# Kernel optimization log

Measured on AMD Instinct MI355X. Metric: run time of the kernel, lower is better.

Reference implementation:

```python
import jax, jax.numpy as jnp
import numpy as np

B, N, D = 1, 4096, 512
H, HD = 8, 64
NBINS = 512
CAND = 64
SCALE = 1.0 / np.sqrt(HD)
MAX_NORM = 1.0 - 1e-5
TWO_PI = 2.0 * np.pi


def _project(x):
    # Poincare-ball style projection: clip L2 norm of each point to MAX_NORM.
    n = jnp.sqrt(jnp.sum(x * x, axis=-1, keepdims=True))
    s = jnp.minimum(1.0, MAX_NORM / jnp.maximum(n, 1e-12))
    return x * s


def _bins(x):
    # Deterministic geometric binning (DavisCache stand-in): quantize the
    # angle of the first two coordinates into NBINS bins.
    ang = jnp.arctan2(x[..., 1], x[..., 0])  # (-pi, pi]
    b = jnp.floor((ang / TWO_PI + 0.5) * NBINS)
    return jnp.clip(b, 0, NBINS - 1).astype(jnp.int32)


def setup_inputs() -> dict:
    key0 = jax.random.key(0)
    ks = jax.random.split(key0, 12)
    w = 0.02  # typical init scale for projection weights
    return {
        "query": jax.random.normal(ks[0], (B, N, D), dtype=jnp.float32),
        "key": jax.random.normal(ks[1], (B, N, D), dtype=jnp.float32),
        "value": jax.random.normal(ks[2], (B, N, D), dtype=jnp.float32),
        "Wq": jax.random.normal(ks[3], (D, D), dtype=jnp.float32) * w,
        "bq": jnp.zeros((D,), dtype=jnp.float32),
        "Wk": jax.random.normal(ks[4], (D, D), dtype=jnp.float32) * w,
        "bk": jnp.zeros((D,), dtype=jnp.float32),
        "Wv": jax.random.normal(ks[5], (D, D), dtype=jnp.float32) * w,
        "bv": jnp.zeros((D,), dtype=jnp.float32),
        "Wo": jax.random.normal(ks[6], (D, D), dtype=jnp.float32) * w,
        "bo": jnp.zeros((D,), dtype=jnp.float32),
    }


def reference(query, key, value, Wq, bq, Wk, bk, Wv, bv, Wo, bo):
    Bq, Nq, Dm = query.shape
    Nk = key.shape[1]
    # projections + split heads -> (B, H, N, HD)
    q = (query @ Wq.T + bq).reshape(Bq, Nq, H, HD).transpose(0, 2, 1, 3)
    k = (key @ Wk.T + bk).reshape(Bq, Nk, H, HD).transpose(0, 2, 1, 3)
    v = (value @ Wv.T + bv).reshape(Bq, Nk, H, HD).transpose(0, 2, 1, 3)
    q = _project(q)
    k = _project(k)

    # geometric binning; candidate keys for a query are those whose bin is
    # within radius 1 of the query's bin (neighboring_bins, radius=1).
    qb = _bins(q)  # (B, H, Nq) int32
    kb = _bins(k)  # (B, H, Nk) int32
    mask = jnp.abs(qb[..., :, None] - kb[..., None, :]) <= 1  # (B,H,Nq,Nk)
    # fallback: if a query has no candidates, attend over all keys
    any_valid = jnp.any(mask, axis=-1, keepdims=True)
    eff = jnp.where(any_valid, mask, True)
    # keep only the first CAND candidates per query (by key index)
    rank = jnp.cumsum(eff.astype(jnp.int32), axis=-1) - 1
    sel = eff & (rank < CAND)

    scores = jnp.einsum("bhqd,bhkd->bhqk", q, k) * SCALE
    scores = jnp.where(sel, scores, -jnp.inf)
    attn = jax.nn.softmax(scores, axis=-1)  # dropout p=0.0 (eval mode)
    out = jnp.einsum("bhqk,bhkd->bhqd", attn, v)

    out = out.transpose(0, 2, 1, 3).reshape(Bq, Nq, Dm)
    return out @ Wo.T + bo
```

## Files before the change

kernel.cpp:

```cpp
#include <hip/hip_runtime.h>
#include <math.h>

typedef unsigned short u16;
typedef __attribute__((ext_vector_type(8))) short v8bf;
typedef __attribute__((ext_vector_type(4))) float f32x4;

#define N_TOK 4096
#define DMODEL 512
#define NHEAD 8
#define HDIM 64
#define CANDN 64
#define NBINS 512
#define BINCAP 64
#define QCAP 128
#define ATT_SCALE 0.125f
#define MAX_NORM_F 0.99999f

__device__ __forceinline__ u16 f2bf(float f) {
  union { float f; unsigned int i; } v; v.f = f;
  unsigned int x = v.i;
  return (u16)((x + 0x7fffu + ((x >> 16) & 1u)) >> 16);
}
__device__ __forceinline__ uint4 pack8v(const float4 x0, const float4 x1) {
  union { u16 h[8]; uint4 u; } r;
  r.h[0] = f2bf(x0.x); r.h[1] = f2bf(x0.y); r.h[2] = f2bf(x0.z); r.h[3] = f2bf(x0.w);
  r.h[4] = f2bf(x1.x); r.h[5] = f2bf(x1.y); r.h[6] = f2bf(x1.z); r.h[7] = f2bf(x1.w);
  return r.u;
}

__global__ __launch_bounds__(256) void fused1_kernel(
    const float* __restrict__ query, const float* __restrict__ key_,
    const float* __restrict__ value,
    const float* __restrict__ Wq, const float* __restrict__ Wk,
    const float* __restrict__ Wv,
    const float* __restrict__ bq, const float* __restrict__ bk,
    const float* __restrict__ bv,
    int* __restrict__ qb, int* __restrict__ kb, unsigned char* __restrict__ flags,
    int* __restrict__ khist,
    u16* __restrict__ Qb, u16* __restrict__ Kb, u16* __restrict__ Vb)
{
  __shared__ __align__(16) char smem[33024];
  const int blk = blockIdx.x;
  const int tid = threadIdx.x;

  if (blk >= 1280) {
    int4 z4; z4.x = 0; z4.y = 0; z4.z = 0; z4.w = 0;
#pragma unroll
    for (int i = 0; i < 8; ++i) ((int4*)khist)[tid + i * 256] = z4;
    return;
  }

  if (blk >= 512) {
    u16* As = (u16*)smem;
    u16* Ws = (u16*)(smem + 10240);

    const int rel = blk - 512;
    const int z = rel >> 8;
    const int rem = rel & 255;
    const int bm = (rem & 63) * 64;
    const int bn = (rem >> 6) * 128;

    const float* X  = (z == 0) ? query : (z == 1) ? key_ : value;
    const float* WF = (z == 0) ? Wq : (z == 1) ? Wk : Wv;
    const float* bias = (z == 0) ? bq : (z == 1) ? bk : bv;
    u16* O          = (z == 0) ? Qb : (z == 1) ? Kb : Vb;

    const int lane = tid & 63;
    const int wave = tid >> 6;
    const int ra  = tid >> 2;
    const int oa  = (tid & 3) * 8;
    const int wm = (wave & 1) * 32;
    const int wn = (wave >> 1) * 64;
    const int l15 = lane & 15;
    const int quad = lane >> 4;

    f32x4 acc[2][4] = {};

    float4 a0f0 = *(const float4*)(X + (bm + ra) * DMODEL + oa);
    float4 a0f1 = *(const float4*)(X + (bm + ra) * DMODEL + oa + 4);
    float4 w0f0 = *(const float4*)(WF + (bn + ra) * DMODEL + oa);
    float4 w0f1 = *(const float4*)(WF + (bn + ra) * DMODEL + oa + 4);
    float4 w1f0 = *(const float4*)(WF + (bn + ra + 64) * DMODEL + oa);
    float4 w1f1 = *(const float4*)(WF + (bn + ra + 64) * DMODEL + oa + 4);

    for (int kt = 0; kt < DMODEL; kt += 32) {
      const int p = (kt >> 5) & 1;
      *(uint4*)&As[p * 2560 + ra * 40 + oa] = pack8v(a0f0, a0f1);
      *(uint4*)&Ws[p * 5120 + ra * 40 + oa] = pack8v(w0f0, w0f1);
      *(uint4*)&Ws[p * 5120 + (ra + 64) * 40 + oa] = pack8v(w1f0, w1f1);
      __syncthreads();
      if (kt + 32 < DMODEL) {
        a0f0 = *(const float4*)(X + (bm + ra) * DMODEL + kt + 32 + oa);
        a0f1 = *(const float4*)(X + (bm + ra) * DMODEL + kt + 32 + oa + 4);
        w0f0 = *(const float4*)(WF + (bn + ra) * DMODEL + kt + 32 + oa);
        w0f1 = *(const float4*)(WF + (bn + ra) * DMODEL + kt + 32 + oa + 4);
        w1f0 = *(const float4*)(WF + (bn + ra + 64) * DMODEL + kt + 32 + oa);
        w1f1 = *(const float4*)(WF + (bn + ra + 64) * DMODEL + kt + 32 + oa + 4);
      }
      v8bf af[2], bfr[4];
#pragma unroll
      for (int i = 0; i < 2; ++i)
        af[i] = *(const v8bf*)&As[p * 2560 + (wm + i * 16 + l15) * 40 + quad * 8];
#pragma unroll
      for (int j = 0; j < 4; ++j)
        bfr[j] = *(const v8bf*)&Ws[p * 5120 + (wn + j * 16 + l15) * 40 + quad * 8];
#pragma unroll
      for (int i = 0; i < 2; ++i)
#pragma unroll
        for (int j = 0; j < 4; ++j)
          acc[i][j] = __builtin_amdgcn_mfma_f32_16x16x32_bf16(af[i], bfr[j], acc[i][j], 0, 0, 0);
    }

    float bval[4];
#pragma unroll
    for (int j = 0; j < 4; ++j) bval[j] = bias[bn + wn + j * 16 + l15];
    const int h = (bn + wn) >> 6;

#pragma unroll
    for (int i = 0; i < 2; ++i) {
#pragma unroll
      for (int r = 0; r < 4; ++r) {
        const int row = bm + wm + i * 16 + quad * 4 + r;
        float v0 = acc[i][0][r] + bval[0];
        float v1 = acc[i][1][r] + bval[1];
        float v2 = acc[i][2][r] + bval[2];
        float v3 = acc[i][3][r] + bval[3];
        if (z != 2) {
          float ss = v0 * v0 + v1 * v1 + v2 * v2 + v3 * v3;
#pragma unroll
          for (int o = 1; o < 16; o <<= 1) ss += __shfl_xor(ss, o);
          const float s = fminf(1.0f, MAX_NORM_F / fmaxf(sqrtf(ss), 1e-12f));
          v0 *= s; v1 *= s; v2 *= s; v3 *= s;
        }
        const int base = (((h << 12) + row) << 6) + l15;
        O[base +  0] = f2bf(v0); O[base + 16] = f2bf(v1);
        O[base + 32] = f2bf(v2); O[base + 48] = f2bf(v3);
      }
    }
    return;
  }

  float* xs = (float*)smem;
  const int isk  = blk >> 8;
  const int tile = blk & 255;
  const float* X = isk ? key_ : query;
  const float* W = isk ? Wk : Wq;

#pragma unroll
  for (int i = 0; i < 8; ++i) {
    const int flat = i * 1024 + tid * 4;
    const int row = flat >> 9, col = flat & 511;
    *(float4*)&xs[row * 516 + col] = *(const float4*)(X + (tile * 16 + row) * DMODEL + col);
  }
  __syncthreads();

  const int n_local = tid >> 4;
  const int pair = tid & 15;
  const int h = pair >> 1, coord = pair & 1;
  const float* wrow = W + ((h << 6) + coord) * DMODEL;
  const float* xrow = &xs[n_local * 516];

  double c0 = 0.0, c1 = 0.0, c2 = 0.0, c3 = 0.0;
  for (int k = 0; k < DMODEL; k += 4) {
    const float4 xv = *(const float4*)(xrow + k);
    const float4 wv = *(const float4*)(wrow + k);
    c0 = fma((double)xv.x, (double)wv.x, c0);
    c1 = fma((double)xv.y, (double)wv.y, c1);
    c2 = fma((double)xv.z, (double)wv.z, c2);
    c3 = fma((double)xv.w, (double)wv.w, c3);
  }
  const double a = (c0 + c1) + (c2 + c3);
  const double other = __shfl_xor(a, 1);
  if (coord == 0) {
    const double a0 = a, a1 = other;
    const int n = tile * 16 + n_local;
    double ang = atan2(a1, a0);
    double t = (ang / 6.283185307179586 + 0.5) * 512.0;
    int b = (int)floor(t);
    b = b < 0 ? 0 : (b > 511 ? 511 : b);
    (isk ? kb : qb)[(h << 12) + n] = b;

    const double r = sqrt(a0 * a0 + a1 * a1);
    const double dist = fabs(t - nearbyint(t));
    const double margin = fmin(0.45, 3.3e-4 / fmax(r, 1e-30) + 5e-5);
    flags[(isk << 15) | (h << 12) | n] = (dist < margin) ? 1 : 0;
  }
}

__device__ float fdlibm_atanf(float x) {
#pragma clang fp contract(off)
  const float atanhi[4] = {4.6364760399e-01f, 7.8539812565e-01f,
                           9.8279368877e-01f, 1.5707962513e+00f};
  const float atanlo[4] = {5.0121582440e-09f, 3.7748947079e-08f,
                           3.4473217170e-08f, 7.5497894159e-08f};
  const float aT[5] = {3.3333328366e-01f, -1.9999158382e-01f, 1.4253635705e-01f,
                       -1.0648017377e-01f, 6.1687607318e-02f};
  unsigned ix = __float_as_uint(x);
  const unsigned sign = ix >> 31;
  ix &= 0x7fffffffu;
  int id;
  float z, w, s1, s2;
  if (ix >= 0x4c800000u) {
    z = atanhi[3] + 0x1p-120f;
    return sign ? -z : z;
  }
  if (ix < 0x3ee00000u) {
    if (ix < 0x39800000u) return x;
    id = -1;
  } else {
    x = fabsf(x);
    if (ix < 0x3f980000u) {
      if (ix < 0x3f300000u) { id = 0; x = (2.0f * x - 1.0f) / (2.0f + x); }
      else                  { id = 1; x = (x - 1.0f) / (x + 1.0f); }
    } else {
      if (ix < 0x401c0000u) { id = 2; x = (x - 1.5f) / (1.0f + 1.5f * x); }
      else                  { id = 3; x = -1.0f / x; }
    }
  }
  z = x * x;
  w = z * z;
  s1 = z * (aT[0] + w * (aT[2] + w * aT[4]));
  s2 = w * (aT[1] + w * aT[3]);
  if (id < 0) return x - x * (s1 + s2);
  z = atanhi[id] - ((x * (s1 + s2) - atanlo[id]) - x);
  return sign ? -z : z;
}

__device__ float fdlibm_atan2f(float y, float x) {
#pragma clang fp contract(off)
  const float pi = 3.1415927410e+00f, pi_lo = -8.7422776573e-08f;
  const unsigned hx = __float_as_uint(x), hy = __float_as_uint(y);
  if (hx == 0x3f800000u) return fdlibm_atanf(y);
  const unsigned m = ((hy >> 31) & 1u) | ((hx >> 30) & 2u);
  const unsigned ix = hx & 0x7fffffffu, iy = hy & 0x7fffffffu;
  if (iy == 0u) {
    switch (m) { case 0: case 1: return y; case 2: return pi; default: return -pi; }
  }
  if (ix == 0u) return (m & 1u) ? -1.57079637050628662f : 1.57079637050628662f;
  float z;
  if (ix + (26u << 23) < iy) {
    z = 1.57079637050628662f;
    return (m & 1u) ? -z : z;
  }
  if ((m & 2u) && iy + (26u << 23) < ix) z = 0.0f;
  else z = fdlibm_atanf(fabsf(y / x));
  switch (m) {
    case 0: return z;
    case 1: return -z;
    case 2: return pi - (z - pi_lo);
    default: return (z - pi_lo) - pi;
  }
}

__global__ __launch_bounds__(256) void binfix_kernel(
    const float* __restrict__ query, const float* __restrict__ key_,
    const float* __restrict__ Wq, const float* __restrict__ Wk,
    const unsigned char* __restrict__ flags,
    int* __restrict__ qb, int* __restrict__ kb)
{
  __shared__ int wle[64];
  __shared__ int wlc;

  const int tid = threadIdx.x;
  const int slice = blockIdx.x;

  if (tid == 0) wlc = 0;
  __syncthreads();
  if (tid < 128) {
    const int flat = (slice << 7) + tid;
    if (flags[flat]) {
      const int p = atomicAdd(&wlc, 1);
      if (p < 64) wle[p] = flat;
    }
  }
  __syncthreads();
  int nw = wlc; if (nw > 64) nw = 64;
  const int w = tid >> 6, d = tid & 63;
  for (int e = w; e < nw; e += 4) {
    const int flat = wle[e];
    const int n = flat & 4095;
    const int h = (flat >> 12) & 7;
    const int isk = flat >> 15;
    const float* xr = (isk ? key_ : query) + n * DMODEL;
    const float* wr = (isk ? Wk : Wq) + ((h << 6) + d) * DMODEL;
    float acc = 0.0f;
    for (int k = 0; k < DMODEL; k += 16) {
      const float4 xa = *(const float4*)(xr + k);
      const float4 xb = *(const float4*)(xr + k + 4);
      const float4 xc = *(const float4*)(xr + k + 8);
      const float4 xd = *(const float4*)(xr + k + 12);
      const float4 wa = *(const float4*)(wr + k);
      const float4 wb = *(const float4*)(wr + k + 4);
      const float4 wc = *(const float4*)(wr + k + 8);
      const float4 wd = *(const float4*)(wr + k + 12);
      acc = __fmaf_rn(xa.x, wa.x, acc); acc = __fmaf_rn(xa.y, wa.y, acc);
      acc = __fmaf_rn(xa.z, wa.z, acc); acc = __fmaf_rn(xa.w, wa.w, acc);
      acc = __fmaf_rn(xb.x, wb.x, acc); acc = __fmaf_rn(xb.y, wb.y, acc);
      acc = __fmaf_rn(xb.z, wb.z, acc); acc = __fmaf_rn(xb.w, wb.w, acc);
      acc = __fmaf_rn(xc.x, wc.x, acc); acc = __fmaf_rn(xc.y, wc.y, acc);
      acc = __fmaf_rn(xc.z, wc.z, acc); acc = __fmaf_rn(xc.w, wc.w, acc);
      acc = __fmaf_rn(xd.x, wd.x, acc); acc = __fmaf_rn(xd.y, wd.y, acc);
      acc = __fmaf_rn(xd.z, wd.z, acc); acc = __fmaf_rn(xd.w, wd.w, acc);
    }
    {
#pragma clang fp contract(off)
      const float sq = acc * acc;
      float rr[8];
#pragma unroll
      for (int j = 0; j < 8; ++j) rr[j] = __shfl(sq, j);
      for (int i = 8; i < 64; i += 8) {
#pragma unroll
        for (int j = 0; j < 8; ++j) rr[j] += __shfl(sq, i + j);
      }
      const float ss = ((rr[0] + rr[1]) + (rr[2] + rr[3])) +
                       ((rr[4] + rr[5]) + (rr[6] + rr[7]));
      const float nrm = __fsqrt_rn(ss);
      const float s = fminf(1.0f, 0.99999f / fmaxf(nrm, 1e-12f));
      const float c0 = __shfl(acc, 0) * s;
      const float c1 = __shfl(acc, 1) * s;
      const float cr = (float)atan2((double)c1, (double)c0);
      const float fd = fdlibm_atan2f(c1, c0);
      const float tol = fmaxf(fabsf(cr) * 6e-7f, 1e-30f);
      const float ang = (fabsf(fd - cr) <= tol) ? fd : cr;
      const float t = ((ang / 6.2831854820251465f) + 0.5f) * 512.0f;
      int b = (int)floorf(t);
      b = b < 0 ? 0 : (b > 511 ? 511 : b);
      if (d == 0) (isk ? kb : qb)[(h << 12) + n] = b;
    }
  }
}

__global__ __launch_bounds__(256) void bin_hist_kernel(
    const int* __restrict__ kb, const int* __restrict__ qb,
    int* __restrict__ khist, u16* __restrict__ blist,
    int* __restrict__ qhist, u16* __restrict__ qlist)
{
  const int h = blockIdx.x;
  const int type = blockIdx.y;
  const int* src = type ? qb : kb;
  int* hist = type ? qhist : khist;
  u16* list = type ? qlist : blist;
  const int cap = type ? QCAP : BINCAP;

  const int i = blockIdx.z * 256 + threadIdx.x;
  const int b = src[(h << 12) + i];
  const int pos = atomicAdd(&hist[(h << 9) + b], 1);
  if (pos < cap) list[((h << 9) + b) * cap + pos] = (u16)i;
}

__global__ __launch_bounds__(64) void attn_bin_kernel(
    const u16* __restrict__ Qb, const u16* __restrict__ Kb,
    const u16* __restrict__ Vb, const int* __restrict__ qhist,
    const u16* __restrict__ qlist, const int* __restrict__ khist,
    const u16* __restrict__ blist, u16* __restrict__ aout)
{
  __shared__ u16 kf[4 * 2 * 4 * 16 * 8];
  __shared__ u16 vf[4 * 2 * 4 * 16 * 8];
  __shared__ u16 pf[16 * 72];
  __shared__ u16 s_cand[64];
  __shared__ int s_qg[16];

  const int hb = blockIdx.x;
  const int h = hb >> 9;
  const int b = hb & 511;
  int qcnt = qhist[hb];
  if (qcnt > QCAP) qcnt = QCAP;
  if (qcnt == 0) return;

  const int lane = threadIdx.x;
  const int l15 = lane & 15;
  const int quad = lane >> 4;

  int v0 = 0xFFFF, v1 = 0xFFFF, v2 = 0xFFFF;
  int c0 = 0, c1 = 0, c2 = 0;
  if (b > 0) {
    c0 = khist[(h << 9) + b - 1];
    if (c0 > BINCAP) c0 = BINCAP;
    if (lane < c0) v0 = (int)blist[(((h << 9) + b - 1) << 6) + lane];
  }
  {
    c1 = khist[(h << 9) + b];
    if (c1 > BINCAP) c1 = BINCAP;
    if (lane < c1) v1 = (int)blist[(((h << 9) + b) << 6) + lane];
  }
  if (b < NBINS - 1) {
    c2 = khist[(h << 9) + b + 1];
    if (c2 > BINCAP) c2 = BINCAP;
    if (lane < c2) v2 = (int)blist[(((h << 9) + b + 1) << 6) + lane];
  }

  int r0 = 0, r1 = 0, r2 = 0;
#pragma unroll 8
  for (int j = 0; j < 64; ++j) {
    const int w0 = __shfl(v0, j);
    const int w1 = __shfl(v1, j);
    const int w2 = __shfl(v2, j);
    r0 += (w0 < v0) + (w1 < v0) + (w2 < v0);
    r1 += (w0 < v1) + (w1 < v1) + (w2 < v1);
    r2 += (w0 < v2) + (w1 < v2) + (w2 < v2);
  }
  const int tot = c0 + c1 + c2;
  const int ccnt = tot < CANDN ? tot : CANDN;
  const int ccnt_eff = (tot == 0) ? 64 : ccnt;
  if (tot == 0) {
    s_cand[lane] = (u16)lane;
  } else {
    if (v0 != 0xFFFF && r0 < CANDN) s_cand[r0] = (u16)v0;
    if (v1 != 0xFFFF && r1 < CANDN) s_cand[r1] = (u16)v1;
    if (v2 != 0xFFFF && r2 < CANDN) s_cand[r2] = (u16)v2;
  }
  __syncthreads();
  if (tot > 0 && lane >= ccnt) s_cand[lane] = s_cand[0];
  __syncthreads();

  {
    const int r = lane >> 3, s = lane & 7;
    const int ks = s >> 2, qd = s & 3;
#pragma unroll
    for (int it = 0; it < 8; ++it) {
      const int key = it * 8 + r;
      const int c = s_cand[key];
      const uint4 kv = *(const uint4*)(Kb + ((h << 18) | (c << 6)) + s * 8);
      const int idx = ((((key >> 4) * 2 + ks) * 4 + qd) * 16 + (key & 15)) * 8;
      *(uint4*)&kf[idx] = kv;
    }
  }
  {
    const int r = lane >> 3, s = lane & 7;
    const int nt = s >> 1, d0 = (s & 1) * 8;
#pragma unroll
    for (int it = 0; it < 8; ++it) {
      const int key = it * 8 + r;
      const int c = s_cand[key];
      union { u16 hh[8]; uint4 u; } vv;
      vv.u = *(const uint4*)(Vb + ((h << 18) | (c << 6)) + s * 8);
      const int kstep = key >> 5, qd = (key >> 3) & 3, j = key & 7;
#pragma unroll
      for (int m = 0; m < 8; ++m)
        vf[(((nt * 2 + kstep) * 4 + qd) * 16 + d0 + m) * 8 + j] = vv.hh[m];
    }
  }
  __syncthreads();

  v8bf akf[4][2], bvf[4][2];
#pragma unroll
  for (int t = 0; t < 4; ++t)
#pragma unroll
    for (int ks = 0; ks < 2; ++ks) {
      akf[t][ks] = *(const v8bf*)&kf[(((t * 2 + ks) * 4 + quad) * 16 + l15) * 8];
      bvf[t][ks] = *(const v8bf*)&vf[(((t * 2 + ks) * 4 + quad) * 16 + l15) * 8];
    }

  const int nchunk = (qcnt + 15) >> 4;
  for (int ci = 0; ci < nchunk; ++ci) {
    const int base = ci << 4;
    const int qcn = min(16, qcnt - base);
    __syncthreads();
    if (lane < 16) {
      int idx = base + lane;
      if (idx > qcnt - 1) idx = qcnt - 1;
      s_qg[lane] = (int)qlist[(hb << 7) + idx];
    }
    __syncthreads();

    const u16* qrow = Qb + ((h << 18) | (s_qg[l15] << 6));
    v8bf bq[2];
#pragma unroll
    for (int ks = 0; ks < 2; ++ks)
      bq[ks] = *(const v8bf*)(qrow + ks * 32 + quad * 8);

    float sc[16];
    __builtin_amdgcn_s_setprio(1);
#pragma unroll
    for (int t = 0; t < 4; ++t) {
      f32x4 sa = {0.f, 0.f, 0.f, 0.f};
      sa = __builtin_amdgcn_mfma_f32_16x16x32_bf16(akf[t][0], bq[0], sa, 0, 0, 0);
      sa = __builtin_amdgcn_mfma_f32_16x16x32_bf16(akf[t][1], bq[1], sa, 0, 0, 0);
#pragma unroll
      for (int r = 0; r < 4; ++r) {
        const int key = t * 16 + quad * 4 + r;
        sc[t * 4 + r] = (key < ccnt_eff) ? sa[r] * ATT_SCALE : -INFINITY;
      }
    }
    __builtin_amdgcn_s_setprio(0);
    float mx = sc[0];
#pragma unroll
    for (int i = 1; i < 16; ++i) mx = fmaxf(mx, sc[i]);
    mx = fmaxf(mx, __shfl_xor(mx, 16));
    mx = fmaxf(mx, __shfl_xor(mx, 32));
    float sum = 0.0f;
    float pe[16];
#pragma unroll
    for (int i = 0; i < 16; ++i) { pe[i] = __expf(sc[i] - mx); sum += pe[i]; }
    sum += __shfl_xor(sum, 16);
    sum += __shfl_xor(sum, 32);
    const float inv = 1.0f / sum;

    __syncthreads();
#pragma unroll
    for (int t = 0; t < 4; ++t)
#pragma unroll
      for (int r = 0; r < 4; ++r)
        pf[l15 * 72 + t * 16 + quad * 4 + r] = f2bf(pe[t * 4 + r] * inv);
    __syncthreads();

    v8bf ap[2];
#pragma unroll
    for (int ks = 0; ks < 2; ++ks)
      ap[ks] = *(const v8bf*)&pf[l15 * 72 + ks * 32 + quad * 8];

    __builtin_amdgcn_s_setprio(1);
#pragma unroll
    for (int nt = 0; nt < 4; ++nt) {
      f32x4 o = {0.f, 0.f, 0.f, 0.f};
      o = __builtin_amdgcn_mfma_f32_16x16x32_bf16(ap[0], bvf[nt][0], o, 0, 0, 0);
      o = __builtin_amdgcn_mfma_f32_16x16x32_bf16(ap[1], bvf[nt][1], o, 0, 0, 0);
#pragma unroll
      for (int r = 0; r < 4; ++r) {
        const int row = quad * 4 + r;
        if (row < qcn)
          aout[s_qg[row] * DMODEL + (h << 6) + nt * 16 + l15] = f2bf(o[r]);
      }
    }
    __builtin_amdgcn_s_setprio(0);
  }
}

__global__ __launch_bounds__(256) void gemm_out_kernel(
    const u16* __restrict__ A, const float* __restrict__ WF,
    const float* __restrict__ bias, float* __restrict__ O)
{
  __shared__ u16 As[2][64 * 40];
  __shared__ u16 Ws[2][64 * 40];

  const int tid  = threadIdx.x;
  const int lane = tid & 63;
  const int wave = tid >> 6;
  const int ra  = tid >> 2;
  const int oa  = (tid & 3) * 8;

  const int bm = blockIdx.x * 64;
  const int bn = blockIdx.y * 64;
  const int wm = (wave & 1) * 32;
  const int wn = (wave >> 1) * 32;
  const int l15 = lane & 15;
  const int quad = lane >> 4;

  f32x4 acc[2][2] = {};

  uint4 a0 = *(const uint4*)(A + (bm + ra) * DMODEL + oa);
  float4 w0f0 = *(const float4*)(WF + (bn + ra) * DMODEL + oa);
  float4 w0f1 = *(const float4*)(WF + (bn + ra) * DMODEL + oa + 4);

  for (int kt = 0; kt < DMODEL; kt += 32) {
    const int p = (kt >> 5) & 1;
    *(uint4*)&As[p][ra * 40 + oa] = a0;
    *(uint4*)&Ws[p][ra * 40 + oa] = pack8v(w0f0, w0f1);
    __syncthreads();
    if (kt + 32 < DMODEL) {
      a0 = *(const uint4*)(A + (bm + ra) * DMODEL + kt + 32 + oa);
      w0f0 = *(const float4*)(WF + (bn + ra) * DMODEL + kt + 32 + oa);
      w0f1 = *(const float4*)(WF + (bn + ra) * DMODEL + kt + 32 + oa + 4);
    }
    v8bf af[2], bfr[2];
#pragma unroll
    for (int i = 0; i < 2; ++i)
      af[i] = *(const v8bf*)&As[p][(wm + i * 16 + l15) * 40 + quad * 8];
#pragma unroll
    for (int j = 0; j < 2; ++j)
      bfr[j] = *(const v8bf*)&Ws[p][(wn + j * 16 + l15) * 40 + quad * 8];
#pragma unroll
    for (int i = 0; i < 2; ++i)
#pragma unroll
      for (int j = 0; j < 2; ++j)
        acc[i][j] = __builtin_amdgcn_mfma_f32_16x16x32_bf16(af[i], bfr[j], acc[i][j], 0, 0, 0);
  }

#pragma unroll
  for (int j = 0; j < 2; ++j) {
    const int cg = bn + wn + j * 16 + l15;
    const float bval = bias[cg];
#pragma unroll
    for (int i = 0; i < 2; ++i) {
      const int rbase = bm + wm + i * 16 + quad * 4;
#pragma unroll
      for (int r = 0; r < 4; ++r)
        O[(rbase + r) * DMODEL + cg] = acc[i][j][r] + bval;
    }
  }
}

extern "C" void kernel_launch(void* const* d_in, const int* in_sizes, int n_in,
                              void* d_out, int out_size, void* d_ws, size_t ws_size,
                              hipStream_t stream) {
  const float* query = (const float*)d_in[0];
  const float* key_  = (const float*)d_in[1];
  const float* value = (const float*)d_in[2];
  const float* Wq = (const float*)d_in[3];
  const float* bq = (const float*)d_in[4];
  const float* Wk = (const float*)d_in[5];
  const float* bk = (const float*)d_in[6];
  const float* Wv = (const float*)d_in[7];
  const float* bv = (const float*)d_in[8];
  const float* Wo = (const float*)d_in[9];
  const float* bo = (const float*)d_in[10];

  char* ws = (char*)d_ws;
  u16* Qb    = (u16*)(ws + 14680064);
  u16* Kb    = (u16*)(ws + 18874368);
  u16* Vb    = (u16*)(ws + 23068672);
  u16* aout  = (u16*)(ws + 27262976);
  int* qb    = (int*)(ws + 31457280);
  int* kb    = (int*)(ws + 31588352);
  unsigned char* flags = (unsigned char*)(ws + 31719424);
  int* khist = (int*)(ws + 31784960);
  int* qhist = (int*)(ws + 31801344);
  u16* blist = (u16*)(ws + 31817728);
  u16* qlist = (u16*)(ws + 32342016);

  fused1_kernel<<<1281, 256, 0, stream>>>(
      query, key_, value, Wq, Wk, Wv, bq, bk, bv,
      qb, kb, flags, khist, Qb, Kb, Vb);
  binfix_kernel<<<512, 256, 0, stream>>>(
      query, key_, Wq, Wk, flags, qb, kb);
  bin_hist_kernel<<<dim3(8, 2, 16), 256, 0, stream>>>(
      kb, qb, khist, blist, qhist, qlist);
  attn_bin_kernel<<<4096, 64, 0, stream>>>(
      Qb, Kb, Vb, qhist, qlist, khist, blist, aout);
  gemm_out_kernel<<<dim3(64, 8), 256, 0, stream>>>(aout, Wo, bo, (float*)d_out);
}
```

Before: 200.7 us.

## Move QKV GEMM into bin-fix kernel and alias K/V shared buffers in attention

The fused first kernel now only computes the fast bin estimates and clears the histogram. The QKV projection GEMM moves into the bin-fix kernel, so the small bin-fix blocks run alongside the GEMM instead of in a separate launch after it. In the attention kernel, K fragments are loaded into registers before V is staged into the same shared buffer, which drops the separate V buffer to reduce LDS use and possibly raise occupancy, at the cost of extra barriers. The work per launch changes balance, and the bin kernel, which uses a large shared array, now runs alone.

```diff
diff --git a/kernel.cpp b/kernel.cpp
--- a/kernel.cpp
+++ b/kernel.cpp
@@ -28,119 +28,23 @@
   return r.u;
 }
 
-__global__ __launch_bounds__(256) void fused1_kernel(
+__global__ __launch_bounds__(256) void bins_kernel(
     const float* __restrict__ query, const float* __restrict__ key_,
-    const float* __restrict__ value,
     const float* __restrict__ Wq, const float* __restrict__ Wk,
-    const float* __restrict__ Wv,
-    const float* __restrict__ bq, const float* __restrict__ bk,
-    const float* __restrict__ bv,
-    int* __restrict__ qb, int* __restrict__ kb, unsigned char* __restrict__ flags,
-    int* __restrict__ khist,
-    u16* __restrict__ Qb, u16* __restrict__ Kb, u16* __restrict__ Vb)
+    int* __restrict__ qb, int* __restrict__ kb,
+    unsigned char* __restrict__ flags, int* __restrict__ khist)
 {
-  __shared__ __align__(16) char smem[33024];
+  __shared__ float xs[16 * 516];
   const int blk = blockIdx.x;
   const int tid = threadIdx.x;
 
-  if (blk >= 1280) {
+  if (blk >= 512) {
     int4 z4; z4.x = 0; z4.y = 0; z4.z = 0; z4.w = 0;
 #pragma unroll
     for (int i = 0; i < 8; ++i) ((int4*)khist)[tid + i * 256] = z4;
     return;
   }
 
-  if (blk >= 512) {
-    u16* As = (u16*)smem;
-    u16* Ws = (u16*)(smem + 10240);
-
-    const int rel = blk - 512;
-    const int z = rel >> 8;
-    const int rem = rel & 255;
-    const int bm = (rem & 63) * 64;
-    const int bn = (rem >> 6) * 128;
-
-    const float* X  = (z == 0) ? query : (z == 1) ? key_ : value;
-    const float* WF = (z == 0) ? Wq : (z == 1) ? Wk : Wv;
-    const float* bias = (z == 0) ? bq : (z == 1) ? bk : bv;
-    u16* O          = (z == 0) ? Qb : (z == 1) ? Kb : Vb;
-
-    const int lane = tid & 63;
-    const int wave = tid >> 6;
-    const int ra  = tid >> 2;
-    const int oa  = (tid & 3) * 8;
-    const int wm = (wave & 1) * 32;
-    const int wn = (wave >> 1) * 64;
-    const int l15 = lane & 15;
-    const int quad = lane >> 4;
-
-    f32x4 acc[2][4] = {};
-
-    float4 a0f0 = *(const float4*)(X + (bm + ra) * DMODEL + oa);
-    float4 a0f1 = *(const float4*)(X + (bm + ra) * DMODEL + oa + 4);
-    float4 w0f0 = *(const float4*)(WF + (bn + ra) * DMODEL + oa);
-    float4 w0f1 = *(const float4*)(WF + (bn + ra) * DMODEL + oa + 4);
-    float4 w1f0 = *(const float4*)(WF + (bn + ra + 64) * DMODEL + oa);
-    float4 w1f1 = *(const float4*)(WF + (bn + ra + 64) * DMODEL + oa + 4);
-
-    for (int kt = 0; kt < DMODEL; kt += 32) {
-      const int p = (kt >> 5) & 1;
-      *(uint4*)&As[p * 2560 + ra * 40 + oa] = pack8v(a0f0, a0f1);
-      *(uint4*)&Ws[p * 5120 + ra * 40 + oa] = pack8v(w0f0, w0f1);
-      *(uint4*)&Ws[p * 5120 + (ra + 64) * 40 + oa] = pack8v(w1f0, w1f1);
-      __syncthreads();
-      if (kt + 32 < DMODEL) {
-        a0f0 = *(const float4*)(X + (bm + ra) * DMODEL + kt + 32 + oa);
-        a0f1 = *(const float4*)(X + (bm + ra) * DMODEL + kt + 32 + oa + 4);
-        w0f0 = *(const float4*)(WF + (bn + ra) * DMODEL + kt + 32 + oa);
-        w0f1 = *(const float4*)(WF + (bn + ra) * DMODEL + kt + 32 + oa + 4);
-        w1f0 = *(const float4*)(WF + (bn + ra + 64) * DMODEL + kt + 32 + oa);
-        w1f1 = *(const float4*)(WF + (bn + ra + 64) * DMODEL + kt + 32 + oa + 4);
-      }
-      v8bf af[2], bfr[4];
-#pragma unroll
-      for (int i = 0; i < 2; ++i)
-        af[i] = *(const v8bf*)&As[p * 2560 + (wm + i * 16 + l15) * 40 + quad * 8];
-#pragma unroll
-      for (int j = 0; j < 4; ++j)
-        bfr[j] = *(const v8bf*)&Ws[p * 5120 + (wn + j * 16 + l15) * 40 + quad * 8];
-#pragma unroll
-      for (int i = 0; i < 2; ++i)
-#pragma unroll
-        for (int j = 0; j < 4; ++j)
-          acc[i][j] = __builtin_amdgcn_mfma_f32_16x16x32_bf16(af[i], bfr[j], acc[i][j], 0, 0, 0);
-    }
-
-    float bval[4];
-#pragma unroll
-    for (int j = 0; j < 4; ++j) bval[j] = bias[bn + wn + j * 16 + l15];
-    const int h = (bn + wn) >> 6;
-
-#pragma unroll
-    for (int i = 0; i < 2; ++i) {
-#pragma unroll
-      for (int r = 0; r < 4; ++r) {
-        const int row = bm + wm + i * 16 + quad * 4 + r;
-        float v0 = acc[i][0][r] + bval[0];
-        float v1 = acc[i][1][r] + bval[1];
-        float v2 = acc[i][2][r] + bval[2];
-        float v3 = acc[i][3][r] + bval[3];
-        if (z != 2) {
-          float ss = v0 * v0 + v1 * v1 + v2 * v2 + v3 * v3;
-#pragma unroll
-          for (int o = 1; o < 16; o <<= 1) ss += __shfl_xor(ss, o);
-          const float s = fminf(1.0f, MAX_NORM_F / fmaxf(sqrtf(ss), 1e-12f));
-          v0 *= s; v1 *= s; v2 *= s; v3 *= s;
-        }
-        const int base = (((h << 12) + row) << 6) + l15;
-        O[base +  0] = f2bf(v0); O[base + 16] = f2bf(v1);
-        O[base + 32] = f2bf(v2); O[base + 48] = f2bf(v3);
-      }
-    }
-    return;
-  }
-
-  float* xs = (float*)smem;
   const int isk  = blk >> 8;
   const int tile = blk & 255;
   const float* X = isk ? key_ : query;
@@ -252,80 +156,177 @@
   }
 }
 
-__global__ __launch_bounds__(256) void binfix_kernel(
+__global__ __launch_bounds__(256) void fixgemm_kernel(
     const float* __restrict__ query, const float* __restrict__ key_,
+    const float* __restrict__ value,
     const float* __restrict__ Wq, const float* __restrict__ Wk,
+    const float* __restrict__ Wv,
+    const float* __restrict__ bq, const float* __restrict__ bk,
+    const float* __restrict__ bv,
     const unsigned char* __restrict__ flags,
-    int* __restrict__ qb, int* __restrict__ kb)
+    int* __restrict__ qb, int* __restrict__ kb,
+    u16* __restrict__ Qb, u16* __restrict__ Kb, u16* __restrict__ Vb)
 {
+  __shared__ __align__(16) char smem[30720];
   __shared__ int wle[64];
   __shared__ int wlc;
 
+  const int blk = blockIdx.x;
   const int tid = threadIdx.x;
-  const int slice = blockIdx.x;
-
-  if (tid == 0) wlc = 0;
-  __syncthreads();
-  if (tid < 128) {
-    const int flat = (slice << 7) + tid;
-    if (flags[flat]) {
-      const int p = atomicAdd(&wlc, 1);
-      if (p < 64) wle[p] = flat;
-    }
-  }
-  __syncthreads();
-  int nw = wlc; if (nw > 64) nw = 64;
-  const int w = tid >> 6, d = tid & 63;
-  for (int e = w; e < nw; e += 4) {
-    const int flat = wle[e];
-    const int n = flat & 4095;
-    const int h = (flat >> 12) & 7;
-    const int isk = flat >> 15;
-    const float* xr = (isk ? key_ : query) + n * DMODEL;
-    const float* wr = (isk ? Wk : Wq) + ((h << 6) + d) * DMODEL;
-    float acc = 0.0f;
-    for (int k = 0; k < DMODEL; k += 16) {
-      const float4 xa = *(const float4*)(xr + k);
-      const float4 xb = *(const float4*)(xr + k + 4);
-      const float4 xc = *(const float4*)(xr + k + 8);
-      const float4 xd = *(const float4*)(xr + k + 12);
-      const float4 wa = *(const float4*)(wr + k);
-      const float4 wb = *(const float4*)(wr + k + 4);
-      const float4 wc = *(const float4*)(wr + k + 8);
-      const float4 wd = *(const float4*)(wr + k + 12);
-      acc = __fmaf_rn(xa.x, wa.x, acc); acc = __fmaf_rn(xa.y, wa.y, acc);
-      acc = __fmaf_rn(xa.z, wa.z, acc); acc = __fmaf_rn(xa.w, wa.w, acc);
-      acc = __fmaf_rn(xb.x, wb.x, acc); acc = __fmaf_rn(xb.y, wb.y, acc);
-      acc = __fmaf_rn(xb.z, wb.z, acc); acc = __fmaf_rn(xb.w, wb.w, acc);
-      acc = __fmaf_rn(xc.x, wc.x, acc); acc = __fmaf_rn(xc.y, wc.y, acc);
-      acc = __fmaf_rn(xc.z, wc.z, acc); acc = __fmaf_rn(xc.w, wc.w, acc);
-      acc = __fmaf_rn(xd.x, wd.x, acc); acc = __fmaf_rn(xd.y, wd.y, acc);
-      acc = __fmaf_rn(xd.z, wd.z, acc); acc = __fmaf_rn(xd.w, wd.w, acc);
-    }
-    {
+
+  if (blk < 512) {
+    const int slice = blk;
+    if (tid == 0) wlc = 0;
+    __syncthreads();
+    if (tid < 128) {
+      const int flat = (slice << 7) + tid;
+      if (flags[flat]) {
+        const int p = atomicAdd(&wlc, 1);
+        if (p < 64) wle[p] = flat;
+      }
+    }
+    __syncthreads();
+    int nw = wlc; if (nw > 64) nw = 64;
+    const int w = tid >> 6, d = tid & 63;
+    for (int e = w; e < nw; e += 4) {
+      const int flat = wle[e];
+      const int n = flat & 4095;
+      const int h = (flat >> 12) & 7;
+      const int isk = flat >> 15;
+      const float* xr = (isk ? key_ : query) + n * DMODEL;
+      const float* wr = (isk ? Wk : Wq) + ((h << 6) + d) * DMODEL;
+      float acc = 0.0f;
+      for (int k = 0; k < DMODEL; k += 16) {
+        const float4 xa = *(const float4*)(xr + k);
+        const float4 xb = *(const float4*)(xr + k + 4);
+        const float4 xc = *(const float4*)(xr + k + 8);
+        const float4 xd = *(const float4*)(xr + k + 12);
+        const float4 wa = *(const float4*)(wr + k);
+        const float4 wb = *(const float4*)(wr + k + 4);
+        const float4 wc = *(const float4*)(wr + k + 8);
+        const float4 wd = *(const float4*)(wr + k + 12);
+        acc = __fmaf_rn(xa.x, wa.x, acc); acc = __fmaf_rn(xa.y, wa.y, acc);
+        acc = __fmaf_rn(xa.z, wa.z, acc); acc = __fmaf_rn(xa.w, wa.w, acc);
+        acc = __fmaf_rn(xb.x, wb.x, acc); acc = __fmaf_rn(xb.y, wb.y, acc);
+        acc = __fmaf_rn(xb.z, wb.z, acc); acc = __fmaf_rn(xb.w, wb.w, acc);
+        acc = __fmaf_rn(xc.x, wc.x, acc); acc = __fmaf_rn(xc.y, wc.y, acc);
+        acc = __fmaf_rn(xc.z, wc.z, acc); acc = __fmaf_rn(xc.w, wc.w, acc);
+        acc = __fmaf_rn(xd.x, wd.x, acc); acc = __fmaf_rn(xd.y, wd.y, acc);
+        acc = __fmaf_rn(xd.z, wd.z, acc); acc = __fmaf_rn(xd.w, wd.w, acc);
+      }
+      {
 #pragma clang fp contract(off)
-      const float sq = acc * acc;
-      float rr[8];
-#pragma unroll
-      for (int j = 0; j < 8; ++j) rr[j] = __shfl(sq, j);
-      for (int i = 8; i < 64; i += 8) {
-#pragma unroll
-        for (int j = 0; j < 8; ++j) rr[j] += __shfl(sq, i + j);
+        const float sq = acc * acc;
+        float rr[8];
+#pragma unroll
+        for (int j = 0; j < 8; ++j) rr[j] = __shfl(sq, j);
+        for (int i = 8; i < 64; i += 8) {
+#pragma unroll
+          for (int j = 0; j < 8; ++j) rr[j] += __shfl(sq, i + j);
+        }
+        const float ss = ((rr[0] + rr[1]) + (rr[2] + rr[3])) +
+                         ((rr[4] + rr[5]) + (rr[6] + rr[7]));
+        const float nrm = __fsqrt_rn(ss);
+        const float s = fminf(1.0f, 0.99999f / fmaxf(nrm, 1e-12f));
+        const float c0 = __shfl(acc, 0) * s;
+        const float c1 = __shfl(acc, 1) * s;
+        const float cr = (float)atan2((double)c1, (double)c0);
+        const float fd = fdlibm_atan2f(c1, c0);
+        const float tol = fmaxf(fabsf(cr) * 6e-7f, 1e-30f);
+        const float ang = (fabsf(fd - cr) <= tol) ? fd : cr;
+        const float t = ((ang / 6.2831854820251465f) + 0.5f) * 512.0f;
+        int b = (int)floorf(t);
+        b = b < 0 ? 0 : (b > 511 ? 511 : b);
+        if (d == 0) (isk ? kb : qb)[(h << 12) + n] = b;
       }
-      const float ss = ((rr[0] + rr[1]) + (rr[2] + rr[3])) +
-                       ((rr[4] + rr[5]) + (rr[6] + rr[7]));
-      const float nrm = __fsqrt_rn(ss);
-      const float s = fminf(1.0f, 0.99999f / fmaxf(nrm, 1e-12f));
-      const float c0 = __shfl(acc, 0) * s;
-      const float c1 = __shfl(acc, 1) * s;
-      const float cr = (float)atan2((double)c1, (double)c0);
-      const float fd = fdlibm_atan2f(c1, c0);
-      const float tol = fmaxf(fabsf(cr) * 6e-7f, 1e-30f);
-      const float ang = (fabsf(fd - cr) <= tol) ? fd : cr;
-      const float t = ((ang / 6.2831854820251465f) + 0.5f) * 512.0f;
-      int b = (int)floorf(t);
-      b = b < 0 ? 0 : (b > 511 ? 511 : b);
-      if (d == 0) (isk ? kb : qb)[(h << 12) + n] = b;
+    }
+    return;
+  }
+
+  u16* As = (u16*)smem;
+  u16* Ws = (u16*)(smem + 10240);
+
+  const int rel = blk - 512;
+  const int z = rel >> 8;
+  const int rem = rel & 255;
+  const int bm = (rem & 63) * 64;
+  const int bn = (rem >> 6) * 128;
+
+  const float* X  = (z == 0) ? query : (z == 1) ? key_ : value;
+  const float* WF = (z == 0) ? Wq : (z == 1) ? Wk : Wv;
+  const float* bias = (z == 0) ? bq : (z == 1) ? bk : bv;
+  u16* O          = (z == 0) ? Qb : (z == 1) ? Kb : Vb;
+
+  const int lane = tid & 63;
+  const int wave = tid >> 6;
+  const int ra  = tid >> 2;
+  const int oa  = (tid & 3) * 8;
+  const int wm = (wave & 1) * 32;
+  const int wn = (wave >> 1) * 64;
+  const int l15 = lane & 15;
+  const int quad = lane >> 4;
+
+  f32x4 acc[2][4] = {};
+
+  float4 a0f0 = *(const float4*)(X + (bm + ra) * DMODEL + oa);
+  float4 a0f1 = *(const float4*)(X + (bm + ra) * DMODEL + oa + 4);
+  float4 w0f0 = *(const float4*)(WF + (bn + ra) * DMODEL + oa);
+  float4 w0f1 = *(const float4*)(WF + (bn + ra) * DMODEL + oa + 4);
+  float4 w1f0 = *(const float4*)(WF + (bn + ra + 64) * DMODEL + oa);
+  float4 w1f1 = *(const float4*)(WF + (bn + ra + 64) * DMODEL + oa + 4);
+
+  for (int kt = 0; kt < DMODEL; kt += 32) {
+    const int p = (kt >> 5) & 1;
+    *(uint4*)&As[p * 2560 + ra * 40 + oa] = pack8v(a0f0, a0f1);
+    *(uint4*)&Ws[p * 5120 + ra * 40 + oa] = pack8v(w0f0, w0f1);
+    *(uint4*)&Ws[p * 5120 + (ra + 64) * 40 + oa] = pack8v(w1f0, w1f1);
+    __syncthreads();
+    if (kt + 32 < DMODEL) {
+      a0f0 = *(const float4*)(X + (bm + ra) * DMODEL + kt + 32 + oa);
+      a0f1 = *(const float4*)(X + (bm + ra) * DMODEL + kt + 32 + oa + 4);
+      w0f0 = *(const float4*)(WF + (bn + ra) * DMODEL + kt + 32 + oa);
+      w0f1 = *(const float4*)(WF + (bn + ra) * DMODEL + kt + 32 + oa + 4);
+      w1f0 = *(const float4*)(WF + (bn + ra + 64) * DMODEL + kt + 32 + oa);
+      w1f1 = *(const float4*)(WF + (bn + ra + 64) * DMODEL + kt + 32 + oa + 4);
+    }
+    v8bf af[2], bfr[4];
+#pragma unroll
+    for (int i = 0; i < 2; ++i)
+      af[i] = *(const v8bf*)&As[p * 2560 + (wm + i * 16 + l15) * 40 + quad * 8];
+#pragma unroll
+    for (int j = 0; j < 4; ++j)
+      bfr[j] = *(const v8bf*)&Ws[p * 5120 + (wn + j * 16 + l15) * 40 + quad * 8];
+#pragma unroll
+    for (int i = 0; i < 2; ++i)
+#pragma unroll
+      for (int j = 0; j < 4; ++j)
+        acc[i][j] = __builtin_amdgcn_mfma_f32_16x16x32_bf16(af[i], bfr[j], acc[i][j], 0, 0, 0);
+  }
+
+  float bval[4];
+#pragma unroll
+  for (int j = 0; j < 4; ++j) bval[j] = bias[bn + wn + j * 16 + l15];
+  const int h = (bn + wn) >> 6;
+
+#pragma unroll
+  for (int i = 0; i < 2; ++i) {
+#pragma unroll
+    for (int r = 0; r < 4; ++r) {
+      const int row = bm + wm + i * 16 + quad * 4 + r;
+      float v0 = acc[i][0][r] + bval[0];
+      float v1 = acc[i][1][r] + bval[1];
+      float v2 = acc[i][2][r] + bval[2];
+      float v3 = acc[i][3][r] + bval[3];
+      if (z != 2) {
+        float ss = v0 * v0 + v1 * v1 + v2 * v2 + v3 * v3;
+#pragma unroll
+        for (int o = 1; o < 16; o <<= 1) ss += __shfl_xor(ss, o);
+        const float s = fminf(1.0f, MAX_NORM_F / fmaxf(sqrtf(ss), 1e-12f));
+        v0 *= s; v1 *= s; v2 *= s; v3 *= s;
+      }
+      const int base = (((h << 12) + row) << 6) + l15;
+      O[base +  0] = f2bf(v0); O[base + 16] = f2bf(v1);
+      O[base + 32] = f2bf(v2); O[base + 48] = f2bf(v3);
     }
   }
 }
@@ -355,7 +356,6 @@
     const u16* __restrict__ blist, u16* __restrict__ aout)
 {
   __shared__ u16 kf[4 * 2 * 4 * 16 * 8];
-  __shared__ u16 vf[4 * 2 * 4 * 16 * 8];
   __shared__ u16 pf[16 * 72];
   __shared__ u16 s_cand[64];
   __shared__ int s_qg[16];
@@ -425,6 +425,15 @@
       *(uint4*)&kf[idx] = kv;
     }
   }
+  __syncthreads();
+  v8bf akf[4][2];
+#pragma unroll
+  for (int t = 0; t < 4; ++t)
+#pragma unroll
+    for (int ks = 0; ks < 2; ++ks)
+      akf[t][ks] = *(const v8bf*)&kf[(((t * 2 + ks) * 4 + quad) * 16 + l15) * 8];
+  __syncthreads();
+
   {
     const int r = lane >> 3, s = lane & 7;
     const int nt = s >> 1, d0 = (s & 1) * 8;
@@ -437,19 +446,16 @@
       const int kstep = key >> 5, qd = (key >> 3) & 3, j = key & 7;
 #pragma unroll
       for (int m = 0; m < 8; ++m)
-        vf[(((nt * 2 + kstep) * 4 + qd) * 16 + d0 + m) * 8 + j] = vv.hh[m];
+        kf[(((nt * 2 + kstep) * 4 + qd) * 16 + d0 + m) * 8 + j] = vv.hh[m];
     }
   }
   __syncthreads();
-
-  v8bf akf[4][2], bvf[4][2];
+  v8bf bvf[4][2];
 #pragma unroll
   for (int t = 0; t < 4; ++t)
 #pragma unroll
-    for (int ks = 0; ks < 2; ++ks) {
-      akf[t][ks] = *(const v8bf*)&kf[(((t * 2 + ks) * 4 + quad) * 16 + l15) * 8];
-      bvf[t][ks] = *(const v8bf*)&vf[(((t * 2 + ks) * 4 + quad) * 16 + l15) * 8];
-    }
+    for (int ks = 0; ks < 2; ++ks)
+      bvf[t][ks] = *(const v8bf*)&kf[(((t * 2 + ks) * 4 + quad) * 16 + l15) * 8];
 
   const int nchunk = (qcnt + 15) >> 4;
   for (int ci = 0; ci < nchunk; ++ci) {
@@ -618,11 +624,11 @@
   u16* blist = (u16*)(ws + 31817728);
   u16* qlist = (u16*)(ws + 32342016);
 
-  fused1_kernel<<<1281, 256, 0, stream>>>(
+  bins_kernel<<<513, 256, 0, stream>>>(
+      query, key_, Wq, Wk, qb, kb, flags, khist);
+  fixgemm_kernel<<<1280, 256, 0, stream>>>(
       query, key_, value, Wq, Wk, Wv, bq, bk, bv,
-      qb, kb, flags, khist, Qb, Kb, Vb);
-  binfix_kernel<<<512, 256, 0, stream>>>(
-      query, key_, Wq, Wk, flags, qb, kb);
+      flags, qb, kb, Qb, Kb, Vb);
   bin_hist_kernel<<<dim3(8, 2, 16), 256, 0, stream>>>(
       kb, qb, khist, blist, qhist, qlist);
   attn_bin_kernel<<<4096, 64, 0, stream>>>(
```

New measurement: 194.9 us. 1.03x faster.
